# Optimization experiments

Measured on AMD Instinct MI355X. Metric: run time of the kernel, lower is better.

## Reference

```python
import jax, jax.numpy as jnp
import numpy as np

FP8_MAX = 448.0   # e4m3 max finite value
BLOCK = 128


def _cast_e4m3(v):
    """Fake-cast to fp8 e4m3: round to nearest representable value (3 mantissa bits,
    min normal exponent -6, subnormal step 2^-9), saturate at +-448."""
    a = jnp.minimum(jnp.abs(v), FP8_MAX)
    e = jnp.floor(jnp.log2(jnp.maximum(a, jnp.float32(2.0) ** -9)))
    e = jnp.maximum(e, -6.0)                 # subnormal range
    step = jnp.exp2(e - 3.0)                 # 3 mantissa bits
    q = jnp.round(a / step) * step
    q = jnp.minimum(q, FP8_MAX)
    return jnp.sign(v) * q


def fake_quant_blockwise(x, br, bc):
    """Per-(br x bc)-tile scale = amax/448, cast to e4m3, dequantize."""
    R, C = x.shape
    xt = x.reshape(R // br, br, C // bc, bc)
    amax = jnp.max(jnp.abs(xt), axis=(1, 3), keepdims=True)
    scale = jnp.maximum(amax, 1e-12) / FP8_MAX
    q = _cast_e4m3(xt / scale) * scale
    return q.reshape(R, C)


def setup_inputs() -> dict:
    key = jax.random.key(0)
    k1, k2 = jax.random.split(key)
    x = jax.random.normal(k1, (8192, 4096), dtype=jnp.float32)
    weight = jax.random.normal(k2, (4096, 4096), dtype=jnp.float32) * 0.02
    bias = jnp.zeros((4096,), dtype=jnp.float32)
    return {"x": x, "weight": weight, "bias": bias}


def reference(x, weight, bias):
    # activations: per-row 1x128 blocks (is_left); weight: 128x128 square tiles (is_sqtile)
    x_fq = fake_quant_blockwise(x, 1, BLOCK)
    w_fq = fake_quant_blockwise(weight, BLOCK, BLOCK)
    return jnp.einsum('ti,oi->to', x_fq, w_fq) + bias
```

## Files before the change

kernel.cpp:

```cpp
#include <hip/hip_runtime.h>

#define M_DIM 8192
#define N_DIM 4096
#define K_DIM 4096

typedef __bf16 bf16x8 __attribute__((ext_vector_type(8)));
typedef float f32x4 __attribute__((ext_vector_type(4)));

__device__ __forceinline__ unsigned short f2bf(float f) {
    unsigned u = __float_as_uint(f);
    u += 0x7FFFu + ((u >> 16) & 1u);
    return (unsigned short)(u >> 16);
}

__device__ __forceinline__ float cast_e4m3(float v) {
    float a = fminf(fabsf(v), 448.0f);
    float am = fmaxf(a, 0x1p-9f);
    int e = (int)((__float_as_uint(am) >> 23) & 0xFFu) - 127;
    e = (e < -6) ? -6 : e;
    float step = __uint_as_float((unsigned)(e - 3 + 127) << 23);
    float q = rintf(a / step) * step;
    q = fminf(q, 448.0f);
    return (v < 0.0f) ? -q : q;
}

__global__ __launch_bounds__(256) void quant_x(const float* __restrict__ X,
                                               unsigned short* __restrict__ Xq) {
    const int g = threadIdx.x >> 5;
    const int l = threadIdx.x & 31;
    const long rb = (long)blockIdx.x * 8 + g;
    const int row = (int)(rb >> 5);
    const int kb = (int)(rb & 31);
    const size_t base = (size_t)row * K_DIM + kb * 128 + l * 4;
    const float4 v = *(const float4*)&X[base];
    float amax = fmaxf(fmaxf(fabsf(v.x), fabsf(v.y)), fmaxf(fabsf(v.z), fabsf(v.w)));
    #pragma unroll
    for (int m = 16; m >= 1; m >>= 1)
        amax = fmaxf(amax, __shfl_xor(amax, m));
    const float scale = fmaxf(amax, 1e-12f) / 448.0f;
    ushort4 o;
    o.x = f2bf(cast_e4m3(v.x / scale) * scale);
    o.y = f2bf(cast_e4m3(v.y / scale) * scale);
    o.z = f2bf(cast_e4m3(v.z / scale) * scale);
    o.w = f2bf(cast_e4m3(v.w / scale) * scale);
    *(ushort4*)&Xq[base] = o;
}

__global__ __launch_bounds__(256) void quant_w(const float* __restrict__ W,
                                               unsigned short* __restrict__ Wq) {
    const int tile = blockIdx.x;
    const int tr = tile >> 5;
    const int tc = tile & 31;
    const int t = threadIdx.x;
    const int c4 = (t & 31) * 4;
    const float* base = W + (size_t)(tr * 128) * K_DIM + tc * 128;

    float4 v[16];
    float amax = 0.0f;
    #pragma unroll
    for (int p = 0; p < 16; ++p) {
        const int r = p * 8 + (t >> 5);
        v[p] = *(const float4*)&base[(size_t)r * K_DIM + c4];
        amax = fmaxf(amax, fmaxf(fmaxf(fabsf(v[p].x), fabsf(v[p].y)),
                                 fmaxf(fabsf(v[p].z), fabsf(v[p].w))));
    }
    #pragma unroll
    for (int m = 32; m >= 1; m >>= 1)
        amax = fmaxf(amax, __shfl_xor(amax, m));
    __shared__ float red[4];
    if ((t & 63) == 0) red[t >> 6] = amax;
    __syncthreads();
    const float am4 = fmaxf(fmaxf(red[0], red[1]), fmaxf(red[2], red[3]));
    const float scale = fmaxf(am4, 1e-12f) / 448.0f;

    unsigned short* out = Wq + (size_t)(tr * 128) * K_DIM + tc * 128;
    #pragma unroll
    for (int p = 0; p < 16; ++p) {
        const int r = p * 8 + (t >> 5);
        ushort4 o;
        o.x = f2bf(cast_e4m3(v[p].x / scale) * scale);
        o.y = f2bf(cast_e4m3(v[p].y / scale) * scale);
        o.z = f2bf(cast_e4m3(v[p].z / scale) * scale);
        o.w = f2bf(cast_e4m3(v[p].w / scale) * scale);
        *(ushort4*)&out[(size_t)r * K_DIM + c4] = o;
    }
}

#define GLOAD16(g, l)                                                          \
    __builtin_amdgcn_global_load_lds(                                          \
        (const __attribute__((address_space(1))) void*)(g),                    \
        (__attribute__((address_space(3))) void*)(l), 16, 0, 0)


#define BARRIER() __builtin_amdgcn_s_barrier()
#define LGKM0() asm volatile("s_waitcnt lgkmcnt(0)" ::: "memory")
#define LGKM8() asm volatile("s_waitcnt lgkmcnt(8)" ::: "memory")
#define VM6()   asm volatile("s_waitcnt vmcnt(6)" ::: "memory")
#define VM0()   asm volatile("s_waitcnt vmcnt(0)" ::: "memory")

#define STAGE(G, grow0, kt, ebase, ht) do {                                    \
    const int _kt = (kt) > 63 ? 63 : (kt);                                     \
    const unsigned short* _s0 = (G) +                                          \
        (size_t)((grow0) + (ht) * 128 + w * 8 + sr) * K_DIM + _kt * 64 + src_col; \
    const unsigned short* _s1 = _s0 + (size_t)64 * K_DIM;                      \
    char* _lb = (char*)lds + (ebase) * 2 + ((ht) * 128 + w * 8) * 128;         \
    GLOAD16(_s0, _lb);                                                         \
    GLOAD16(_s1, _lb + 8192);                                                  \
} while (0)

#define LDA(mh, ebase) do {                                                    \
    _Pragma("unroll") for (int _m = 0; _m < 4; ++_m) {                         \
        const int _row = wm * 128 + (mh) * 64 + _m * 16 + lr;                  \
        a[_m][0] = *(const bf16x8*)&lds[(ebase) + _row * 64 + ((0  + hk) ^ rsw)]; \
        a[_m][1] = *(const bf16x8*)&lds[(ebase) + _row * 64 + ((32 + hk) ^ rsw)]; \
    }                                                                          \
} while (0)

#define LDB(nh, dst, ebase) do {                                               \
    _Pragma("unroll") for (int _n = 0; _n < 2; ++_n) {                         \
        const int _row = wn * 64 + (nh) * 32 + _n * 16 + lr;                   \
        dst[_n][0] = *(const bf16x8*)&lds[(ebase) + _row * 64 + ((0  + hk) ^ rsw)]; \
        dst[_n][1] = *(const bf16x8*)&lds[(ebase) + _row * 64 + ((32 + hk) ^ rsw)]; \
    }                                                                          \
} while (0)

#define MMA(mh, nh, bb) do {                                                   \
    _Pragma("unroll") for (int _m = 0; _m < 4; ++_m)                           \
    _Pragma("unroll") for (int _n = 0; _n < 2; ++_n)                           \
    _Pragma("unroll") for (int _k = 0; _k < 2; ++_k)                           \
        acc[(mh) * 4 + _m][(nh) * 2 + _n] =                                    \
            __builtin_amdgcn_mfma_f32_16x16x32_bf16(                           \
                a[_m][_k], bb[_n][_k], acc[(mh) * 4 + _m][(nh) * 2 + _n], 0, 0, 0); \
} while (0)

#define PRIO1() __builtin_amdgcn_s_setprio(1)
#define PRIO0() __builtin_amdgcn_s_setprio(0)

__global__ __launch_bounds__(512, 2) void gemm256(const unsigned short* __restrict__ A,
                                                  const unsigned short* __restrict__ B,
                                                  const float* __restrict__ bias,
                                                  float* __restrict__ C) {
    __shared__ __align__(16) unsigned short lds[65536];

    const int t = threadIdx.x;
    const int lane = t & 63;
    const int w = t >> 6;
    const int wm = w >> 2, wn = w & 3;

    int bid = blockIdx.x;
    bid = (bid & 7) * 64 + (bid >> 3);
    const int bm = bid >> 4, bn = bid & 15;
    const size_t brow = (size_t)bm * 256, bcol = (size_t)bn * 256;

    const int sr = lane >> 3;
    const int src_col = (((lane & 7) ^ ((lane >> 3) & 7)) << 3);
    const int lr = lane & 15;
    const int hk = (lane >> 4) * 8;
    const int rsw = (lane & 7) << 3;

    f32x4 acc[8][4] = {};
    bf16x8 a[4][2], b0[2][2], b1[2][2];

    STAGE(A, brow, 0, 0, 0);     STAGE(A, brow, 0, 0, 1);
    STAGE(B, bcol, 0, 32768, 0); STAGE(B, bcol, 0, 32768, 1);
    STAGE(B, bcol, 1, 49152, 0); STAGE(B, bcol, 1, 49152, 1);
    STAGE(A, brow, 1, 16384, 0);
    VM6(); BARRIER();

    for (int u = 0; u < 64; u += 2) {
        LDA(0, 0); LDB(0, b0, 32768); LDB(1, b1, 32768);
        STAGE(A, brow, u + 1, 16384, 1);
        LGKM8();
        BARRIER(); LGKM0();
        PRIO1(); MMA(0, 0, b0); PRIO0();
        BARRIER();
        STAGE(B, bcol, u + 2, 32768, 0);
        BARRIER();
        PRIO1(); MMA(0, 1, b1); PRIO0();
        BARRIER();
        LDA(1, 0);
        STAGE(B, bcol, u + 2, 32768, 1);
        BARRIER(); LGKM0();
        PRIO1(); MMA(1, 1, b1); PRIO0();
        BARRIER();
        STAGE(A, brow, u + 2, 0, 0);
        BARRIER();
        PRIO1(); MMA(1, 0, b0); PRIO0();
        VM6();
        BARRIER();
        LDA(0, 16384); LDB(0, b0, 49152); LDB(1, b1, 49152);
        STAGE(A, brow, u + 2, 0, 1);
        LGKM8();
        BARRIER(); LGKM0();
        PRIO1(); MMA(0, 0, b0); PRIO0();
        BARRIER();
        STAGE(B, bcol, u + 3, 49152, 0);
        BARRIER();
        PRIO1(); MMA(0, 1, b1); PRIO0();
        BARRIER();
        LDA(1, 16384);
        STAGE(B, bcol, u + 3, 49152, 1);
        BARRIER(); LGKM0();
        PRIO1(); MMA(1, 1, b1); PRIO0();
        BARRIER();
        STAGE(A, brow, u + 3, 16384, 0);
        BARRIER();
        PRIO1(); MMA(1, 0, b0); PRIO0();
        VM6();
        BARRIER();
    }

    VM0();

    #pragma unroll
    for (int i = 0; i < 8; ++i) {
        const size_t row_base = brow + wm * 128 + i * 16 + (lane >> 4) * 4;
        #pragma unroll
        for (int j = 0; j < 4; ++j) {
            const size_t col = bcol + wn * 64 + j * 16 + lr;
            const float bv = bias[col];
            #pragma unroll
            for (int jj = 0; jj < 4; ++jj)
                C[(row_base + jj) * (size_t)N_DIM + col] = acc[i][j][jj] + bv;
        }
    }
}

extern "C" void kernel_launch(void* const* d_in, const int* in_sizes, int n_in,
                              void* d_out, int out_size, void* d_ws, size_t ws_size,
                              hipStream_t stream) {
    const float* x = (const float*)d_in[0];
    const float* w = (const float*)d_in[1];
    const float* bias = (const float*)d_in[2];
    float* out = (float*)d_out;

    unsigned short* xq = (unsigned short*)d_ws;
    unsigned short* wq = xq + (size_t)M_DIM * K_DIM;

    quant_x<<<(M_DIM * (K_DIM / 128)) / 8, 256, 0, stream>>>(x, xq);
    quant_w<<<(N_DIM / 128) * (K_DIM / 128), 256, 0, stream>>>(w, wq);
    gemm256<<<(M_DIM / 256) * (N_DIM / 256), 512, 0, stream>>>(xq, wq, bias, out);
}
```

Before: 293.8 us.

## Coarsen GEMM main-loop schedule into two MMA phases per half-iteration

Restructures the ping-pong main loop so each half-iteration issues A and B tile loads in pairs and runs two MMA groups per phase, halving the number of barriers. The prologue no longer prefetches the next A tile, and the wait counter changes from vmcnt 6 to 4. This cuts synchronisation overhead but shortens how far ahead A tiles are loaded, which may expose global load latency and reduce overlap between memory and MFMA work.

```diff
diff --git a/kernel.cpp b/kernel.cpp
--- a/kernel.cpp
+++ b/kernel.cpp
@@ -94,9 +94,10 @@
 
 #define BARRIER() __builtin_amdgcn_s_barrier()
 #define LGKM0() asm volatile("s_waitcnt lgkmcnt(0)" ::: "memory")
-#define LGKM8() asm volatile("s_waitcnt lgkmcnt(8)" ::: "memory")
-#define VM6()   asm volatile("s_waitcnt vmcnt(6)" ::: "memory")
+#define VM4()   asm volatile("s_waitcnt vmcnt(4)" ::: "memory")
 #define VM0()   asm volatile("s_waitcnt vmcnt(0)" ::: "memory")
+#define PRIO1() __builtin_amdgcn_s_setprio(1)
+#define PRIO0() __builtin_amdgcn_s_setprio(0)
 
 #define STAGE(G, grow0, kt, ebase, ht) do {                                    \
     const int _kt = (kt) > 63 ? 63 : (kt);                                     \
@@ -133,9 +134,6 @@
                 a[_m][_k], bb[_n][_k], acc[(mh) * 4 + _m][(nh) * 2 + _n], 0, 0, 0); \
 } while (0)
 
-#define PRIO1() __builtin_amdgcn_s_setprio(1)
-#define PRIO0() __builtin_amdgcn_s_setprio(0)
-
 __global__ __launch_bounds__(512, 2) void gemm256(const unsigned short* __restrict__ A,
                                                   const unsigned short* __restrict__ B,
                                                   const float* __restrict__ bias,
@@ -164,49 +162,31 @@
     STAGE(A, brow, 0, 0, 0);     STAGE(A, brow, 0, 0, 1);
     STAGE(B, bcol, 0, 32768, 0); STAGE(B, bcol, 0, 32768, 1);
     STAGE(B, bcol, 1, 49152, 0); STAGE(B, bcol, 1, 49152, 1);
-    STAGE(A, brow, 1, 16384, 0);
-    VM6(); BARRIER();
+    VM4(); BARRIER();
 
     for (int u = 0; u < 64; u += 2) {
         LDA(0, 0); LDB(0, b0, 32768); LDB(1, b1, 32768);
-        STAGE(A, brow, u + 1, 16384, 1);
-        LGKM8();
-        BARRIER(); LGKM0();
-        PRIO1(); MMA(0, 0, b0); PRIO0();
-        BARRIER();
-        STAGE(B, bcol, u + 2, 32768, 0);
-        BARRIER();
-        PRIO1(); MMA(0, 1, b1); PRIO0();
+        STAGE(A, brow, u + 1, 16384, 0); STAGE(A, brow, u + 1, 16384, 1);
+        BARRIER(); LGKM0();
+        PRIO1(); MMA(0, 0, b0); MMA(0, 1, b1); PRIO0();
         BARRIER();
         LDA(1, 0);
-        STAGE(B, bcol, u + 2, 32768, 1);
-        BARRIER(); LGKM0();
-        PRIO1(); MMA(1, 1, b1); PRIO0();
-        BARRIER();
-        STAGE(A, brow, u + 2, 0, 0);
-        BARRIER();
-        PRIO1(); MMA(1, 0, b0); PRIO0();
-        VM6();
-        BARRIER();
+        STAGE(B, bcol, u + 2, 32768, 0); STAGE(B, bcol, u + 2, 32768, 1);
+        BARRIER(); LGKM0();
+        PRIO1(); MMA(1, 1, b1); MMA(1, 0, b0); PRIO0();
+        VM4();
+        BARRIER();
+
         LDA(0, 16384); LDB(0, b0, 49152); LDB(1, b1, 49152);
-        STAGE(A, brow, u + 2, 0, 1);
-        LGKM8();
-        BARRIER(); LGKM0();
-        PRIO1(); MMA(0, 0, b0); PRIO0();
-        BARRIER();
-        STAGE(B, bcol, u + 3, 49152, 0);
-        BARRIER();
-        PRIO1(); MMA(0, 1, b1); PRIO0();
+        STAGE(A, brow, u + 2, 0, 0); STAGE(A, brow, u + 2, 0, 1);
+        BARRIER(); LGKM0();
+        PRIO1(); MMA(0, 0, b0); MMA(0, 1, b1); PRIO0();
         BARRIER();
         LDA(1, 16384);
-        STAGE(B, bcol, u + 3, 49152, 1);
-        BARRIER(); LGKM0();
-        PRIO1(); MMA(1, 1, b1); PRIO0();
-        BARRIER();
-        STAGE(A, brow, u + 3, 16384, 0);
-        BARRIER();
-        PRIO1(); MMA(1, 0, b0); PRIO0();
-        VM6();
+        STAGE(B, bcol, u + 3, 49152, 0); STAGE(B, bcol, u + 3, 49152, 1);
+        BARRIER(); LGKM0();
+        PRIO1(); MMA(1, 1, b1); MMA(1, 0, b0); PRIO0();
+        VM4();
         BARRIER();
     }
 
```

After: 294.3 us. About the same (+0.2%).
